# Optimization experiments

Measured on AMD Instinct MI355X. Metric: run time of the kernel, lower is better.

The kernel has to match this reference:

```python
import jax, jax.numpy as jnp
import numpy as np

T, B, N, DEG, F_IN, H, C = 48, 32, 96, 8, 16, 128, 500
E = B * N * DEG          # edges per timestep (already batch-offset within [0, B*N))
M = T * B * N            # total nodes across all timesteps
EPS = 1e-5               # BatchNorm eps


def setup_inputs() -> dict:
    key = jax.random.key(0)
    ks = jax.random.split(key, 24)
    rn = lambda k, s: jax.random.normal(k, s, dtype=jnp.float32) * 0.05
    return {
        "x": jax.random.normal(ks[0], (T, B * N, F_IN), dtype=jnp.float32),
        "edge_index": jax.random.randint(ks[1], (T, 2, E), 0, B * N, dtype=jnp.int32),
        "gcn_w0": rn(ks[2], (F_IN, H)),
        "gcn_w12": rn(ks[3], (2, H, H)),
        "gcn_b": rn(ks[4], (3, H)),
        "bn_gamma": jnp.ones((3, H), dtype=jnp.float32),
        "bn_beta": jnp.zeros((3, H), dtype=jnp.float32),
        "bn_mean": rn(ks[5], (3, H)),
        "bn_var": jax.random.uniform(ks[6], (3, H), minval=0.5, maxval=1.5, dtype=jnp.float32),
        "lstm_wih0": rn(ks[7], (2, 4 * H, H)),
        "lstm_whh0": rn(ks[8], (2, 4 * H, H)),
        "lstm_bih0": rn(ks[9], (2, 4 * H)),
        "lstm_bhh0": rn(ks[10], (2, 4 * H)),
        "lstm_wih1": rn(ks[11], (2, 4 * H, 2 * H)),
        "lstm_whh1": rn(ks[12], (2, 4 * H, H)),
        "lstm_bih1": rn(ks[13], (2, 4 * H)),
        "lstm_bhh1": rn(ks[14], (2, 4 * H)),
        "attn_w1": rn(ks[15], (2 * H, H)),
        "attn_b1": rn(ks[16], (H,)),
        "attn_w2": rn(ks[17], (H, 1)),
        "attn_b2": rn(ks[18], (1,)),
        "fc1_w": rn(ks[19], (2 * H, H)),
        "fc1_b": rn(ks[20], (H,)),
        "fc2_w": rn(ks[21], (H, C)),
        "fc2_b": rn(ks[22], (C,)),
    }


def _lstm_dir(x, wih, whh, bih, bhh):
    # x: [T, B, I]; PyTorch gate order i, f, g, o
    pre = jnp.einsum('tbi,gi->tbg', x, wih) + bih  # input projection hoisted out of scan
    h0 = jnp.zeros((x.shape[1], whh.shape[1]), x.dtype)

    def step(carry, p):
        h, c = carry
        g = p + h @ whh.T + bhh
        i, f, gg, o = jnp.split(g, 4, axis=-1)
        c = jax.nn.sigmoid(f) * c + jax.nn.sigmoid(i) * jnp.tanh(gg)
        h = jax.nn.sigmoid(o) * jnp.tanh(c)
        return (h, c), h

    _, hs = jax.lax.scan(step, (h0, h0), pre)
    return hs  # [T, B, Hh]


def _bilstm(x, wih, whh, bih, bhh):
    fwd = _lstm_dir(x, wih[0], whh[0], bih[0], bhh[0])
    bwd = _lstm_dir(x[::-1], wih[1], whh[1], bih[1], bhh[1])[::-1]
    return jnp.concatenate([fwd, bwd], axis=-1)  # [T, B, 2H]


def reference(x, edge_index, gcn_w0, gcn_w12, gcn_b,
              bn_gamma, bn_beta, bn_mean, bn_var,
              lstm_wih0, lstm_whh0, lstm_bih0, lstm_bhh0,
              lstm_wih1, lstm_whh1, lstm_bih1, lstm_bhh1,
              attn_w1, attn_b1, attn_w2, attn_b2,
              fc1_w, fc1_b, fc2_w, fc2_b):
    # Fold timesteps into one big node set by offsetting indices by t*B*N
    off = (jnp.arange(T, dtype=jnp.int32) * (B * N))[:, None]
    src = (edge_index[:, 0] + off).reshape(-1)
    dst = (edge_index[:, 1] + off).reshape(-1)

    # GCN symmetric norm with self-loops: deg counts incoming edges + self-loop
    deg = jax.ops.segment_sum(jnp.ones_like(src, dtype=x.dtype), dst, num_segments=M) + 1.0
    dinv = jax.lax.rsqrt(deg)
    enorm = (dinv[src] * dinv[dst])[:, None]   # per-edge norm
    self_norm = (1.0 / deg)[:, None]           # self-loop norm

    h = x.reshape(M, F_IN)
    for l in range(3):
        W = gcn_w0 if l == 0 else gcn_w12[l - 1]
        hw = h @ W  # GCNConv applies linear first
        z = jax.ops.segment_sum(hw[src] * enorm, dst, num_segments=M) + hw * self_norm + gcn_b[l]
        # BatchNorm1d eval-mode (running stats), then ReLU, residual if shapes match
        z = (z - bn_mean[l]) * (bn_gamma[l] * jax.lax.rsqrt(bn_var[l] + EPS)) + bn_beta[l]
        z = jax.nn.relu(z)
        h = z + h if l > 0 else z  # dropout is identity in eval

    # global_mean_pool per graph (fixed N nodes per graph)
    emb = h.reshape(T, B, N, H).mean(axis=2)  # [T, B, H]

    out1 = _bilstm(emb, lstm_wih0, lstm_whh0, lstm_bih0, lstm_bhh0)
    out2 = _bilstm(out1, lstm_wih1, lstm_whh1, lstm_bih1, lstm_bhh1)
    lstm_out = out2.transpose(1, 0, 2)  # [B, T, 2H]

    a = jnp.tanh(lstm_out @ attn_w1 + attn_b1) @ attn_w2 + attn_b2  # [B, T, 1]
    w = jax.nn.softmax(a, axis=1)
    ws = jnp.sum(lstm_out * w, axis=1)  # [B, 2H]

    y = jax.nn.relu(ws @ fc1_w + fc1_b) @ fc2_w + fc2_b
    return jax.nn.log_softmax(y, axis=1)
```

## Files before the change

### kernel.cpp

```cpp
#include <hip/hip_runtime.h>

#define T_ 48
#define B_ 32
#define N_ 96
#define E_ 24576
#define BN_ (B_*N_)
#define M_ (T_*BN_)
#define FIN_ 16
#define H_ 128
#define C_ 500
#define TE_ (T_*E_)
#define EPS_ 1e-5f

typedef _Float16 f16x8 __attribute__((ext_vector_type(8)));
typedef float    f32x4 __attribute__((ext_vector_type(4)));
typedef _Float16 half2v __attribute__((ext_vector_type(2)));

__device__ __forceinline__ ushort f2h(float f) {
    _Float16 h = (_Float16)f;
    union { _Float16 h; ushort u; } v;
    v.h = h;
    return v.u;
}
__device__ __forceinline__ float h2f(ushort u) {
    union { ushort u; _Float16 h; } v;
    v.u = u;
    return (float)v.h;
}
__device__ __forceinline__ half2v pkfma(unsigned int v, unsigned int w, half2v acc) {
#if __has_builtin(__builtin_elementwise_fma)
    return __builtin_elementwise_fma(__builtin_bit_cast(half2v, v),
                                     __builtin_bit_cast(half2v, w), acc);
#else
    half2v hv = __builtin_bit_cast(half2v, v);
    half2v wv = __builtin_bit_cast(half2v, w);
    acc[0] += hv[0]*wv[0];
    acc[1] += hv[1]*wv[1];
    return acc;
#endif
}
__device__ __forceinline__ float dot2pk(unsigned int hbits, unsigned int wbits, float acc) {
#if __has_builtin(__builtin_amdgcn_fdot2)
    return __builtin_amdgcn_fdot2(__builtin_bit_cast(half2v, hbits),
                                  __builtin_bit_cast(half2v, wbits), acc, false);
#else
    half2v hv = __builtin_bit_cast(half2v, hbits);
    half2v wv = __builtin_bit_cast(half2v, wbits);
    acc = fmaf((float)hv[0], (float)wv[0], acc);
    acc = fmaf((float)hv[1], (float)wv[1], acc);
    return acc;
#endif
}
__device__ __forceinline__ float sigm(float x) {
    return 1.f / (1.f + __expf(-x));
}
__device__ __forceinline__ float ftanh(float x) {
    x = fminf(15.f, fmaxf(-15.f, x));
    float e = __expf(2.f * x);
    return (e - 1.f) / (e + 1.f);
}

#define WPREP_TOTAL (384+1024+4096+16384+16384+65536+65536+131072+262144)
#define WPREP_BLOCKS ((WPREP_TOTAL + 1023) / 1024)
__global__ __launch_bounds__(1024) void csr_wprep_k(
    const int* __restrict__ ei, int* __restrict__ csr_off,
    unsigned int* __restrict__ csr_pk,
    const float* __restrict__ gcn_b, const float* __restrict__ gam,
    const float* __restrict__ bet, const float* __restrict__ mu,
    const float* __restrict__ var,
    float* __restrict__ bn_sc, float* __restrict__ bn_sh,
    const float* __restrict__ bih0, const float* __restrict__ bhh0,
    float* __restrict__ bias0,
    const float* __restrict__ bih1, const float* __restrict__ bhh1,
    float* __restrict__ bias1,
    const float* __restrict__ gcn_w0, const float* __restrict__ gcn_w12,
    ushort* __restrict__ w0t, ushort* __restrict__ w1t, ushort* __restrict__ w2t,
    const float* __restrict__ whh0, const float* __restrict__ whh1,
    unsigned int* __restrict__ wpk0, unsigned int* __restrict__ wpk1,
    const float* __restrict__ wih0, const float* __restrict__ wih1,
    ushort* __restrict__ wih0b, ushort* __restrict__ wih1b)
{
    __shared__ int cnt[BN_];
    __shared__ int cur[BN_];
    __shared__ int scanbuf[1024];
    __shared__ unsigned int pk[E_];
    int tid = threadIdx.x;

    if (blockIdx.x >= T_) {
        int i = (blockIdx.x - T_) * 1024 + tid;
        if (i >= WPREP_TOTAL) return;
        if (i < 384) {
            float sc = gam[i] * rsqrtf(var[i] + EPS_);
            bn_sc[i] = sc;
            bn_sh[i] = gcn_b[i]*sc + bet[i] - mu[i]*sc;
            return;
        }
        i -= 384;
        if (i < 1024) {
            bias0[i] = bih0[i] + bhh0[i];
            bias1[i] = bih1[i] + bhh1[i];
            return;
        }
        i -= 1024;
        if (i < 4096) {
            int e = i & 7, lane = (i >> 3) & 63, ct = i >> 9;
            int k = (lane >> 4)*8 + e;
            int c = ct*16 + (lane & 15);
            w0t[i] = (k < 16) ? f2h(gcn_w0[k*128 + c]) : (ushort)0;
            return;
        }
        i -= 4096;
        if (i < 16384) {
            int e = i & 7, lane = (i >> 3) & 63, kk = (i >> 9) & 3, ct = i >> 11;
            int k = kk*32 + (lane >> 4)*8 + e;
            int c = ct*16 + (lane & 15);
            w1t[i] = f2h(gcn_w12[k*128 + c]);
            return;
        }
        i -= 16384;
        if (i < 16384) {
            int e = i & 7, lane = (i >> 3) & 63, kk = (i >> 9) & 3, ct = i >> 11;
            int k = kk*32 + (lane >> 4)*8 + e;
            int c = ct*16 + (lane & 15);
            w2t[i] = f2h(gcn_w12[16384 + k*128 + c]);
            return;
        }
        i -= 16384;
        if (i < 65536) {
            int dir = i >> 15, r = i & 32767;
            int ab = r >> 14, r2 = r & 16383;
            int q = r2 >> 8, tidw = r2 & 255;
            int hh = tidw >> 1, gp = tidw & 1;
            int g = (2*gp + ab)*128 + hh;
            const float* wr = whh0 + ((long)(dir*512 + g))*128 + 2*q;
            wpk0[i] = (unsigned int)f2h(wr[0]) | ((unsigned int)f2h(wr[1]) << 16);
            return;
        }
        i -= 65536;
        if (i < 65536) {
            int dir = i >> 15, r = i & 32767;
            int ab = r >> 14, r2 = r & 16383;
            int q = r2 >> 8, tidw = r2 & 255;
            int hh = tidw >> 1, gp = tidw & 1;
            int g = (2*gp + ab)*128 + hh;
            const float* wr = whh1 + ((long)(dir*512 + g))*128 + 2*q;
            wpk1[i] = (unsigned int)f2h(wr[0]) | ((unsigned int)f2h(wr[1]) << 16);
            return;
        }
        i -= 65536;
        if (i < 131072) {
            int dir = i >> 16, r = i & 0xFFFF;
            int nt = r >> 11, kk = (r >> 9) & 3, lane = (r >> 3) & 63, e = r & 7;
            int n = nt*16 + (lane & 15);
            int k = kk*32 + (lane >> 4)*8 + e;
            wih0b[i] = f2h(wih0[((long)dir*512 + n)*128 + k]);
            return;
        }
        i -= 131072;
        {
            int dir = i >> 17, r = i & 0x1FFFF;
            int nt = r >> 12, kk = (r >> 9) & 7, lane = (r >> 3) & 63, e = r & 7;
            int n = nt*16 + (lane & 15);
            int k = kk*32 + (lane >> 4)*8 + e;
            wih1b[i] = f2h(wih1[((long)dir*512 + n)*256 + k]);
        }
        return;
    }

    int t = blockIdx.x;

    #pragma unroll
    for (int i = 0; i < 3; i++) cnt[tid + i*1024] = 0;
    __syncthreads();

    const int* srcp = ei + ((long)t*2+0)*E_;
    const int* dstp = ei + ((long)t*2+1)*E_;
    #pragma unroll
    for (int i = 0; i < E_/1024; i++)
        atomicAdd(&cnt[dstp[tid + i*1024]], 1);
    __syncthreads();

    int n0 = tid*3;
    int a = cnt[n0], b = cnt[n0+1], c = cnt[n0+2];
    int tot = a + b + c;
    scanbuf[tid] = tot;
    __syncthreads();
    for (int d = 1; d < 1024; d <<= 1) {
        int add = (tid >= d) ? scanbuf[tid-d] : 0;
        __syncthreads();
        scanbuf[tid] += add;
        __syncthreads();
    }
    int excl = scanbuf[tid] - tot;
    cur[n0] = excl; cur[n0+1] = excl + a; cur[n0+2] = excl + a + b;
    int gbase = t*BN_, ebase = t*E_;
    csr_off[gbase+n0]   = ebase + excl;
    csr_off[gbase+n0+1] = ebase + excl + a;
    csr_off[gbase+n0+2] = ebase + excl + a + b;
    if (t == T_-1 && tid == 0) csr_off[M_] = TE_;
    __syncthreads();

    #pragma unroll
    for (int i = 0; i < E_/1024; i++) {
        int e = tid + i*1024;
        int s = srcp[e], d = dstp[e];
        int pos = atomicAdd(&cur[d], 1);
        float w = rsqrtf((float)cnt[s] + 1.f) * rsqrtf((float)cnt[d] + 1.f);
        pk[pos] = (unsigned int)s | ((unsigned int)f2h(w) << 16);
    }
    __syncthreads();

    uint4* dpk = (uint4*)(csr_pk + ebase);
    const uint4* spk = (const uint4*)pk;
    #pragma unroll
    for (int i = 0; i < E_/4096; i++)
        dpk[tid + i*1024] = spk[tid + i*1024];
}

__global__ __launch_bounds__(512) void gcn_layer_k(
    const ushort* __restrict__ h, const ushort* __restrict__ Wt,
    ushort* __restrict__ Cout,
    const int* __restrict__ csr_off, const unsigned int* __restrict__ csr_pk,
    const float* __restrict__ bnsc, const float* __restrict__ bnsh)
{
    __shared__ ushort agg[64][136];
    int nb = gridDim.x;
    int chunk = nb >> 3;
    int bswz = (blockIdx.x & 7) * chunk + (blockIdx.x >> 3);
    int base = bswz * 64;
    int tbase = (base / BN_) * BN_;
    int wv = threadIdx.x >> 6;
    int lane = threadIdx.x & 63;
    int l2 = lane * 2;

    #pragma unroll
    for (int pass = 0; pass < 4; pass++) {
        int nlA = pass*16 + wv*2;
        int nodeA = __builtin_amdgcn_readfirstlane(base + nlA);
        int e00 = __builtin_amdgcn_readfirstlane(csr_off[nodeA]);
        int e01 = __builtin_amdgcn_readfirstlane(csr_off[nodeA+1]);
        int e11 = __builtin_amdgcn_readfirstlane(csr_off[nodeA+2]);
        int dA = e01 - e00, dB = e11 - e01;
        unsigned int mypkA = (lane < dA) ? csr_pk[e00 + lane] : 0u;
        unsigned int mypkB = (lane < dB) ? csr_pk[e01 + lane] : 0u;
        unsigned int selfA = *(const unsigned int*)(h + (size_t)nodeA*128 + l2);
        unsigned int selfB = *(const unsigned int*)(h + (size_t)(nodeA+1)*128 + l2);

        ushort swA = f2h(1.0f / (float)(dA + 1));
        ushort swB = f2h(1.0f / (float)(dB + 1));
        half2v spA = __builtin_bit_cast(half2v, (unsigned int)(swA * 0x10001u));
        half2v spB = __builtin_bit_cast(half2v, (unsigned int)(swB * 0x10001u));
        half2v a0 = __builtin_bit_cast(half2v, selfA);
        a0[0] *= spA[0]; a0[1] *= spA[1];
        half2v b0 = __builtin_bit_cast(half2v, selfB);
        b0[0] *= spB[0]; b0[1] *= spB[1];
        half2v a1 = {(_Float16)0.f, (_Float16)0.f}, a2 = a1, a3 = a1;
        half2v b1 = a1, b2 = a1, b3 = a1;

        int cA = (dA < 64) ? dA : 64;
        int cB = (dB < 64) ? dB : 64;
        int cA4 = cA & ~3, cB4 = cB & ~3;
        int cm = (cA4 > cB4) ? cA4 : cB4;
        for (int j = 0; j < cm; j += 4) {
            unsigned int pA0, pA1, pA2, pA3, vA0, vA1, vA2, vA3;
            unsigned int pB0, pB1, pB2, pB3, vB0, vB1, vB2, vB3;
            bool qA = (j < cA4), qB = (j < cB4);
            if (qA) {
                pA0 = (unsigned int)__builtin_amdgcn_readlane((int)mypkA, j+0);
                pA1 = (unsigned int)__builtin_amdgcn_readlane((int)mypkA, j+1);
                pA2 = (unsigned int)__builtin_amdgcn_readlane((int)mypkA, j+2);
                pA3 = (unsigned int)__builtin_amdgcn_readlane((int)mypkA, j+3);
                vA0 = *(const unsigned int*)(h + (size_t)(tbase + (int)(pA0 & 0xffffu))*128 + l2);
                vA1 = *(const unsigned int*)(h + (size_t)(tbase + (int)(pA1 & 0xffffu))*128 + l2);
                vA2 = *(const unsigned int*)(h + (size_t)(tbase + (int)(pA2 & 0xffffu))*128 + l2);
                vA3 = *(const unsigned int*)(h + (size_t)(tbase + (int)(pA3 & 0xffffu))*128 + l2);
            }
            if (qB) {
                pB0 = (unsigned int)__builtin_amdgcn_readlane((int)mypkB, j+0);
                pB1 = (unsigned int)__builtin_amdgcn_readlane((int)mypkB, j+1);
                pB2 = (unsigned int)__builtin_amdgcn_readlane((int)mypkB, j+2);
                pB3 = (unsigned int)__builtin_amdgcn_readlane((int)mypkB, j+3);
                vB0 = *(const unsigned int*)(h + (size_t)(tbase + (int)(pB0 & 0xffffu))*128 + l2);
                vB1 = *(const unsigned int*)(h + (size_t)(tbase + (int)(pB1 & 0xffffu))*128 + l2);
                vB2 = *(const unsigned int*)(h + (size_t)(tbase + (int)(pB2 & 0xffffu))*128 + l2);
                vB3 = *(const unsigned int*)(h + (size_t)(tbase + (int)(pB3 & 0xffffu))*128 + l2);
            }
            if (qA) {
                a0 = pkfma(vA0, (pA0 >> 16) * 0x10001u, a0);
                a1 = pkfma(vA1, (pA1 >> 16) * 0x10001u, a1);
                a2 = pkfma(vA2, (pA2 >> 16) * 0x10001u, a2);
                a3 = pkfma(vA3, (pA3 >> 16) * 0x10001u, a3);
            }
            if (qB) {
                b0 = pkfma(vB0, (pB0 >> 16) * 0x10001u, b0);
                b1 = pkfma(vB1, (pB1 >> 16) * 0x10001u, b1);
                b2 = pkfma(vB2, (pB2 >> 16) * 0x10001u, b2);
                b3 = pkfma(vB3, (pB3 >> 16) * 0x10001u, b3);
            }
        }
        for (int j = cA4; j < cA; j++) {
            unsigned int pk0 = (unsigned int)__builtin_amdgcn_readlane((int)mypkA, j);
            unsigned int v = *(const unsigned int*)(h + (size_t)(tbase + (int)(pk0 & 0xffffu))*128 + l2);
            a0 = pkfma(v, (pk0 >> 16) * 0x10001u, a0);
        }
        for (int j = cB4; j < cB; j++) {
            unsigned int pk0 = (unsigned int)__builtin_amdgcn_readlane((int)mypkB, j);
            unsigned int v = *(const unsigned int*)(h + (size_t)(tbase + (int)(pk0 & 0xffffu))*128 + l2);
            b0 = pkfma(v, (pk0 >> 16) * 0x10001u, b0);
        }
        for (int jj = e00 + 64; jj < e01; jj++) {
            unsigned int pk0 = __builtin_amdgcn_readfirstlane(csr_pk[jj]);
            unsigned int v = *(const unsigned int*)(h + (size_t)(tbase + (int)(pk0 & 0xffffu))*128 + l2);
            a0 = pkfma(v, (pk0 >> 16) * 0x10001u, a0);
        }
        for (int jj = e01 + 64; jj < e11; jj++) {
            unsigned int pk0 = __builtin_amdgcn_readfirstlane(csr_pk[jj]);
            unsigned int v = *(const unsigned int*)(h + (size_t)(tbase + (int)(pk0 & 0xffffu))*128 + l2);
            b0 = pkfma(v, (pk0 >> 16) * 0x10001u, b0);
        }
        float ra0 = ((float)a0[0] + (float)a1[0]) + ((float)a2[0] + (float)a3[0]);
        float ra1 = ((float)a0[1] + (float)a1[1]) + ((float)a2[1] + (float)a3[1]);
        float rb0 = ((float)b0[0] + (float)b1[0]) + ((float)b2[0] + (float)b3[0]);
        float rb1 = ((float)b0[1] + (float)b1[1]) + ((float)b2[1] + (float)b3[1]);
        *(unsigned int*)&agg[nlA][l2] =
            (unsigned int)f2h(ra0) | ((unsigned int)f2h(ra1) << 16);
        *(unsigned int*)&agg[nlA+1][l2] =
            (unsigned int)f2h(rb0) | ((unsigned int)f2h(rb1) << 16);
    }
    __syncthreads();

    int l16 = lane & 15, lh = lane >> 4;
    int rowgrp = wv >> 1;
    int chalf = (wv & 1) * 4;
    f32x4 acc[4];
    #pragma unroll
    for (int i = 0; i < 4; i++) acc[i] = (f32x4){0.f, 0.f, 0.f, 0.f};
    #pragma unroll
    for (int kk = 0; kk < 4; kk++) {
        f16x8 af = *reinterpret_cast<const f16x8*>(&agg[rowgrp*16 + l16][kk*32 + lh*8]);
        #pragma unroll
        for (int c4 = 0; c4 < 4; c4++) {
            int ct = chalf + c4;
            f16x8 bfr = *reinterpret_cast<const f16x8*>(
                &Wt[(((long)ct*4 + kk)*64 + lane)*8]);
            acc[c4] = __builtin_amdgcn_mfma_f32_16x16x32_f16(af, bfr, acc[c4], 0, 0, 0);
        }
    }
    __syncthreads();

    #pragma unroll
    for (int c4 = 0; c4 < 4; c4++) {
        int col = (chalf + c4)*16 + l16;
        float sc = bnsc[col], sh = bnsh[col];
        #pragma unroll
        for (int r = 0; r < 4; r++) {
            int rl = rowgrp*16 + lh*4 + r;
            float v = acc[c4][r] * sc + sh;
            agg[rl][col] = f2h(fmaxf(v, 0.f));
        }
    }
    __syncthreads();
    long rowblock = (long)base;
    #pragma unroll
    for (int it = 0; it < 2; it++) {
        int s = it*512 + threadIdx.x;
        int rl = s >> 4, c8 = (s & 15) * 8;
        uint4 v = *(const uint4*)&agg[rl][c8];
        uint4 rv = *(const uint4*)&h[(rowblock + rl)*128 + c8];
        half2v* vv = (half2v*)&v;
        const half2v* rr = (const half2v*)&rv;
        vv[0] += rr[0]; vv[1] += rr[1]; vv[2] += rr[2]; vv[3] += rr[3];
        *(uint4*)&Cout[(rowblock + rl)*128 + c8] = v;
    }
}

__global__ __launch_bounds__(256) void gcn0_k(
    const float* __restrict__ x, const ushort* __restrict__ Wt,
    ushort* __restrict__ Cout,
    const int* __restrict__ csr_off, const unsigned int* __restrict__ csr_pk,
    const float* __restrict__ bnsc, const float* __restrict__ bnsh)
{
    __shared__ ushort agg[64][32];
    __shared__ ushort cl[64][136];
    int tid = threadIdx.x;
    int nl = tid >> 2;
    int fq = tid & 3;
    int f0 = fq*4;
    int node = blockIdx.x*64 + nl;
    int tbase = (node / BN_) * BN_;
    int e0 = csr_off[node], e1 = csr_off[node+1];
    float s = 1.0f / (float)(e1 - e0 + 1);
    float4 sv = *(const float4*)(x + (long)node*16 + f0);
    float a0 = sv.x*s, a1 = sv.y*s, a2 = sv.z*s, a3 = sv.w*s;
    int j = e0;
    for (; j + 4 <= e1; j += 4) {
        unsigned int p0 = csr_pk[j], p1 = csr_pk[j+1], p2 = csr_pk[j+2], p3 = csr_pk[j+3];
        int s0 = tbase + (int)(p0 & 0xffffu), s1 = tbase + (int)(p1 & 0xffffu);
        int s2 = tbase + (int)(p2 & 0xffffu), s3 = tbase + (int)(p3 & 0xffffu);
        float w0 = h2f((ushort)(p0 >> 16)), w1 = h2f((ushort)(p1 >> 16));
        float w2 = h2f((ushort)(p2 >> 16)), w3 = h2f((ushort)(p3 >> 16));
        float4 v0 = *(const float4*)(x + (long)s0*16 + f0);
        float4 v1 = *(const float4*)(x + (long)s1*16 + f0);
        float4 v2 = *(const float4*)(x + (long)s2*16 + f0);
        float4 v3 = *(const float4*)(x + (long)s3*16 + f0);
        a0 += v0.x*w0 + v1.x*w1 + v2.x*w2 + v3.x*w3;
        a1 += v0.y*w0 + v1.y*w1 + v2.y*w2 + v3.y*w3;
        a2 += v0.z*w0 + v1.z*w1 + v2.z*w2 + v3.z*w3;
        a3 += v0.w*w0 + v1.w*w1 + v2.w*w2 + v3.w*w3;
    }
    for (; j < e1; j++) {
        unsigned int pk0 = csr_pk[j];
        int sc = tbase + (int)(pk0 & 0xffffu);
        float en = h2f((ushort)(pk0 >> 16));
        float4 v = *(const float4*)(x + (long)sc*16 + f0);
        a0 += v.x*en; a1 += v.y*en; a2 += v.z*en; a3 += v.w*en;
    }
    agg[nl][f0+0] = f2h(a0);
    agg[nl][f0+1] = f2h(a1);
    agg[nl][f0+2] = f2h(a2);
    agg[nl][f0+3] = f2h(a3);
    agg[nl][16+f0+0] = 0;
    agg[nl][16+f0+1] = 0;
    agg[nl][16+f0+2] = 0;
    agg[nl][16+f0+3] = 0;
    __syncthreads();

    int w = tid >> 6, lane = tid & 63;
    int l16 = lane & 15, lh = lane >> 4;
    f16x8 af = *reinterpret_cast<const f16x8*>(&agg[w*16 + l16][lh*8]);
    f32x4 acc[8];
    #pragma unroll
    for (int i = 0; i < 8; i++) acc[i] = (f32x4){0.f, 0.f, 0.f, 0.f};
    #pragma unroll
    for (int ct = 0; ct < 8; ct++) {
        f16x8 bfr = *reinterpret_cast<const f16x8*>(&Wt[((long)ct*64 + lane)*8]);
        acc[ct] = __builtin_amdgcn_mfma_f32_16x16x32_f16(af, bfr, acc[ct], 0, 0, 0);
    }

    #pragma unroll
    for (int ct = 0; ct < 8; ct++) {
        int col = ct*16 + l16;
        float sc = bnsc[col], sh = bnsh[col];
        #pragma unroll
        for (int r = 0; r < 4; r++) {
            int rl = w*16 + lh*4 + r;
            float v = acc[ct][r] * sc + sh;
            cl[rl][col] = f2h(fmaxf(v, 0.f));
        }
    }
    __syncthreads();
    long rowblock = (long)blockIdx.x * 64;
    #pragma unroll
    for (int it = 0; it < 4; it++) {
        int ss = it*256 + tid;
        int rl = ss >> 4, c8 = (ss & 15) * 8;
        uint4 v = *(const uint4*)&cl[rl][c8];
        *(uint4*)&Cout[(rowblock + rl)*128 + c8] = v;
    }
}

template<int K>
__global__ __launch_bounds__(256) void mm_pre_k(
    const ushort* __restrict__ A, const ushort* __restrict__ Wt_all,
    float* __restrict__ Cout_all, const float* __restrict__ bias_all)
{
    constexpr int KST = K/32;
    int dir = blockIdx.z;
    const ushort* Wt = Wt_all + (size_t)dir * 512 * K;
    float* Cout = Cout_all + (size_t)dir * T_ * B_ * 512;
    const float* bias = bias_all + dir * 512;

    int tid = threadIdx.x;
    int w = tid >> 6, lane = tid & 63;
    int l16 = lane & 15, lh = lane >> 4;
    int row0 = blockIdx.x * 64 + w * 16;
    int nt0 = blockIdx.y * 8;

    f32x4 acc[8];
    #pragma unroll
    for (int i = 0; i < 8; i++) acc[i] = (f32x4){0.f, 0.f, 0.f, 0.f};

    #pragma unroll
    for (int kk = 0; kk < KST; kk++) {
        int ka = kk*32 + lh*8;
        f16x8 af = *reinterpret_cast<const f16x8*>(&A[(long)(row0 + l16)*K + ka]);
        #pragma unroll
        for (int ct = 0; ct < 8; ct++) {
            f16x8 bfr = *reinterpret_cast<const f16x8*>(
                &Wt[(((long)(nt0 + ct)*KST + kk)*64 + lane)*8]);
            acc[ct] = __builtin_amdgcn_mfma_f32_16x16x32_f16(af, bfr, acc[ct], 0, 0, 0);
        }
    }

    #pragma unroll
    for (int ct = 0; ct < 8; ct++) {
        int col = (nt0 + ct)*16 + l16;
        float bv = bias[col];
        int gate = col >> 7, hh = col & 127;
        int colp = (gate & 1)*256 + hh*2 + (gate >> 1);
        #pragma unroll
        for (int r = 0; r < 4; r++) {
            int row = row0 + lh*4 + r;
            Cout[(long)row*512 + colp] = acc[ct][r] + bv;
        }
    }
}


__global__ void meanpool_k(const ushort* __restrict__ h, ushort* __restrict__ embb) {
    int row = blockIdx.x;
    int t = row / B_, b = row - t*B_;
    int hh = threadIdx.x;
    const ushort* base = h + ((long)t*BN_ + b*N_)*H_ + hh;
    float acc = 0.f;
    for (int n = 0; n < N_; n++) acc += h2f(base[(long)n*H_]);
    embb[(long)row*H_ + hh] = f2h(acc * (1.f / N_));
}

__global__ __launch_bounds__(256) void lstm_scan_k(
    const float* __restrict__ pre,
    const unsigned int* __restrict__ wpkbuf,
    float* __restrict__ out,
    ushort* __restrict__ outb)
{
    int dir = blockIdx.x >> 5;
    int b   = blockIdx.x & 31;
    int tid = threadIdx.x;
    int gp  = tid & 1;
    int hh  = tid >> 1;

    __shared__ ushort hbuf[2][H_];
    ((ushort*)hbuf)[tid] = 0;
    float creg = 0.f;

    const unsigned int* wpA = wpkbuf + ((long)dir*2 + 0)*64*256;
    const unsigned int* wpB = wpkbuf + ((long)dir*2 + 1)*64*256;
    unsigned int wA[64], wB[64];
    #pragma unroll
    for (int q = 0; q < 64; q++) {
        wA[q] = wpA[q*256 + tid];
        wB[q] = wpB[q*256 + tid];
    }

    const float* pred = pre + (long)dir * T_ * B_ * 512;
    int t = dir ? (T_ - 1) : 0;
    int tstep = dir ? -1 : 1;
    float pvA = pred[(((long)t*B_ + b)*2 + 0)*256 + tid];
    float pvB = pred[(((long)t*B_ + b)*2 + 1)*256 + tid];
    __syncthreads();

    for (int st = 0; st < T_; st++) {
        int tn = t + tstep;
        tn = (tn < 0) ? 0 : ((tn >= T_) ? T_ - 1 : tn);
        float pvAn = pred[(((long)tn*B_ + b)*2 + 0)*256 + tid];
        float pvBn = pred[(((long)tn*B_ + b)*2 + 1)*256 + tid];

        const uint4* h4 = (const uint4*)hbuf[st & 1];
        float a0 = pvA, a1 = 0.f, a2 = 0.f, a3 = 0.f;
        float c0 = pvB, c1 = 0.f, c2 = 0.f, c3 = 0.f;
        #pragma unroll
        for (int jj = 0; jj < 16; jj++) {
            uint4 hv = h4[jj];
            a0 = dot2pk(hv.x, wA[jj*4+0], a0);
            a1 = dot2pk(hv.y, wA[jj*4+1], a1);
            a2 = dot2pk(hv.z, wA[jj*4+2], a2);
            a3 = dot2pk(hv.w, wA[jj*4+3], a3);
            c0 = dot2pk(hv.x, wB[jj*4+0], c0);
            c1 = dot2pk(hv.y, wB[jj*4+1], c1);
            c2 = dot2pk(hv.z, wB[jj*4+2], c2);
            c3 = dot2pk(hv.w, wB[jj*4+3], c3);
        }
        float sA = (a0 + a1) + (a2 + a3);
        float sB = (c0 + c1) + (c2 + c3);
        float oA = __shfl_xor(sA, 1, 64);
        float oB = __shfl_xor(sB, 1, 64);
        float ig = gp ? oA : sA;
        float fg = gp ? oB : sB;
        float gg = gp ? sA : oA;
        float og = gp ? sB : oB;
        float c = sigm(fg) * creg + sigm(ig) * ftanh(gg);
        float h = sigm(og) * ftanh(c);
        creg = c;
        if (gp == 0) {
            hbuf[(st + 1) & 1][hh] = f2h(h);
            long orow = ((long)t*B_ + b)*256 + dir*H_ + hh;
            if (out)  out[orow] = h;
            if (outb) outb[orow] = f2h(h);
        }
        __syncthreads();
        pvA = pvAn; pvB = pvBn;
        t = tn;
    }
}


__global__ __launch_bounds__(128) void attn_a_k(
    const ushort* __restrict__ out2, const float* __restrict__ w1,
    const float* __restrict__ b1, const float* __restrict__ w2,
    const float* __restrict__ b2v, float* __restrict__ a)
{
    int row = blockIdx.x;
    int j = threadIdx.x;
    const ushort* xr = out2 + (long)row * 256;
    float acc = b1[j];
    for (int k = 0; k < 256; k++) acc += h2f(xr[k]) * w1[k*128 + j];
    float u = tanhf(acc) * w2[j];
    __shared__ float red[128];
    red[j] = u;
    __syncthreads();
    for (int d = 64; d > 0; d >>= 1) {
        if (j < d) red[j] += red[j + d];
        __syncthreads();
    }
    if (j == 0) {
        int t = row / B_, b = row - t*B_;
        a[b*T_ + t] = red[0] + b2v[0];
    }
}

__global__ __launch_bounds__(256) void attn_pool_k(
    const ushort* __restrict__ out2, const float* __restrict__ a,
    float* __restrict__ wsv)
{
    int b = blockIdx.x;
    __shared__ float w[T_];
    if (threadIdx.x == 0) {
        float m = -1e30f;
        for (int t = 0; t < T_; t++) m = fmaxf(m, a[b*T_ + t]);
        float s = 0.f;
        for (int t = 0; t < T_; t++) { float e = __expf(a[b*T_ + t] - m); w[t] = e; s += e; }
        float inv = 1.f / s;
        for (int t = 0; t < T_; t++) w[t] *= inv;
    }
    __syncthreads();
    int h2 = threadIdx.x;
    float acc = 0.f;
    for (int t = 0; t < T_; t++) acc += w[t] * h2f(out2[((long)t*B_ + b)*256 + h2]);
    wsv[b*256 + h2] = acc;
}


__global__ __launch_bounds__(512) void head_k(
    const float* __restrict__ wsv, const float* __restrict__ w1,
    const float* __restrict__ b1, const float* __restrict__ w2,
    const float* __restrict__ b2, float* __restrict__ outp)
{
    int b = blockIdx.x;
    int tid = threadIdx.x;
    __shared__ float r[128];
    __shared__ float y[C_];
    __shared__ float red[512];
    if (tid < 128) {
        float acc = b1[tid];
        for (int k = 0; k < 256; k++) acc += wsv[b*256 + k] * w1[k*128 + tid];
        r[tid] = fmaxf(acc, 0.f);
    }
    __syncthreads();
    for (int c = tid; c < C_; c += 512) {
        float acc = b2[c];
        for (int k = 0; k < 128; k++) acc += r[k] * w2[k*C_ + c];
        y[c] = acc;
    }
    __syncthreads();
    float m = -1e30f;
    for (int c = tid; c < C_; c += 512) m = fmaxf(m, y[c]);
    red[tid] = m;
    __syncthreads();
    for (int d = 256; d > 0; d >>= 1) {
        if (tid < d) red[tid] = fmaxf(red[tid], red[tid + d]);
        __syncthreads();
    }
    m = red[0];
    __syncthreads();
    float s = 0.f;
    for (int c = tid; c < C_; c += 512) s += __expf(y[c] - m);
    red[tid] = s;
    __syncthreads();
    for (int d = 256; d > 0; d >>= 1) {
        if (tid < d) red[tid] += red[tid + d];
        __syncthreads();
    }
    float lse = m + logf(red[0]);
    for (int c = tid; c < C_; c += 512) outp[(long)b*C_ + c] = y[c] - lse;
}


extern "C" void kernel_launch(void* const* d_in, const int* in_sizes, int n_in,
                              void* d_out, int out_size, void* d_ws, size_t ws_size,
                              hipStream_t stream) {
    const float* x        = (const float*)d_in[0];
    const int*   ei       = (const int*)d_in[1];
    const float* gcn_w0   = (const float*)d_in[2];
    const float* gcn_w12  = (const float*)d_in[3];
    const float* gcn_b    = (const float*)d_in[4];
    const float* bn_gamma = (const float*)d_in[5];
    const float* bn_beta  = (const float*)d_in[6];
    const float* bn_mean  = (const float*)d_in[7];
    const float* bn_var   = (const float*)d_in[8];
    const float* wih0     = (const float*)d_in[9];
    const float* whh0     = (const float*)d_in[10];
    const float* bih0     = (const float*)d_in[11];
    const float* bhh0     = (const float*)d_in[12];
    const float* wih1     = (const float*)d_in[13];
    const float* whh1     = (const float*)d_in[14];
    const float* bih1     = (const float*)d_in[15];
    const float* bhh1     = (const float*)d_in[16];
    const float* attn_w1  = (const float*)d_in[17];
    const float* attn_b1  = (const float*)d_in[18];
    const float* attn_w2  = (const float*)d_in[19];
    const float* attn_b2  = (const float*)d_in[20];
    const float* fc1_w    = (const float*)d_in[21];
    const float* fc1_b    = (const float*)d_in[22];
    const float* fc2_w    = (const float*)d_in[23];
    const float* fc2_b    = (const float*)d_in[24];

    char* p = (char*)d_ws;
    auto alloc = [&](size_t bytes) {
        void* r = (void*)p;
        p += (bytes + 255) & ~(size_t)255;
        return r;
    };
    ushort* hbA    = (ushort*)alloc((size_t)M_*H_*2);
    ushort* hbB    = (ushort*)alloc((size_t)M_*H_*2);
    int*   csr_off = (int*)  alloc((size_t)(M_+1)*4);
    unsigned int* csr_pk = (unsigned int*)alloc((size_t)TE_*4);
    float* bn_sc   = (float*)alloc(384*4);
    float* bn_sh   = (float*)alloc(384*4);
    float* bias0   = (float*)alloc(1024*4);
    float* bias1   = (float*)alloc(1024*4);
    ushort* w0t    = (ushort*)alloc((size_t)4096*2);
    ushort* w1t    = (ushort*)alloc((size_t)16384*2);
    ushort* w2t    = (ushort*)alloc((size_t)16384*2);
    unsigned int* wpk0 = (unsigned int*)alloc((size_t)2*64*512*4);
    unsigned int* wpk1 = (unsigned int*)alloc((size_t)2*64*512*4);
    ushort* wih0b  = (ushort*)alloc((size_t)2*512*128*2);
    ushort* wih1b  = (ushort*)alloc((size_t)2*512*256*2);
    ushort* embb   = (ushort*)alloc((size_t)T_*B_*H_*2);
    float* pre     = (float*)alloc((size_t)2*T_*B_*512*4);
    ushort* out1b  = (ushort*)alloc((size_t)T_*B_*256*2);
    ushort* out2b  = (ushort*)alloc((size_t)T_*B_*256*2);
    float* attn_av = (float*)alloc((size_t)B_*T_*4);
    float* wsv     = (float*)alloc((size_t)B_*256*4);

    csr_wprep_k<<<T_ + WPREP_BLOCKS, 1024, 0, stream>>>(
        ei, csr_off, csr_pk,
        gcn_b, bn_gamma, bn_beta, bn_mean, bn_var, bn_sc, bn_sh,
        bih0, bhh0, bias0, bih1, bhh1, bias1,
        gcn_w0, gcn_w12, w0t, w1t, w2t,
        whh0, whh1, wpk0, wpk1,
        wih0, wih1, wih0b, wih1b);

    gcn0_k<<<M_/64, 256, 0, stream>>>(x, w0t, hbA, csr_off, csr_pk,
                                      bn_sc + 0, bn_sh + 0);
    gcn_layer_k<<<M_/64, 512, 0, stream>>>(hbA, w1t, hbB, csr_off, csr_pk,
                                           bn_sc + 128, bn_sh + 128);
    gcn_layer_k<<<M_/64, 512, 0, stream>>>(hbB, w2t, hbA, csr_off, csr_pk,
                                           bn_sc + 256, bn_sh + 256);

    meanpool_k<<<T_*B_, 128, 0, stream>>>(hbA, embb);

    mm_pre_k<128><<<dim3((T_*B_)/64, 4, 2), 256, 0, stream>>>(embb, wih0b, pre, bias0);
    lstm_scan_k<<<64, 256, 0, stream>>>(pre, wpk0, nullptr, out1b);

    mm_pre_k<256><<<dim3((T_*B_)/64, 4, 2), 256, 0, stream>>>(out1b, wih1b, pre, bias1);
    lstm_scan_k<<<64, 256, 0, stream>>>(pre, wpk1, nullptr, out2b);

    attn_a_k<<<T_*B_, 128, 0, stream>>>(out2b, attn_w1, attn_b1, attn_w2, attn_b2, attn_av);
    attn_pool_k<<<B_, 256, 0, stream>>>(out2b, attn_av, wsv);

    head_k<<<B_, 512, 0, stream>>>(wsv, fc1_w, fc1_b, fc2_w, fc2_b, (float*)d_out);
}
```

Baseline: 270.5 us.

## Fuse attention scoring, softmax pooling and classifier head into one kernel

```diff
diff --git a/kernel.cpp b/kernel.cpp
--- a/kernel.cpp
+++ b/kernel.cpp
@@ -593,72 +593,72 @@
     }
 }
 
-
-__global__ __launch_bounds__(128) void attn_a_k(
-    const ushort* __restrict__ out2, const float* __restrict__ w1,
-    const float* __restrict__ b1, const float* __restrict__ w2,
-    const float* __restrict__ b2v, float* __restrict__ a)
-{
-    int row = blockIdx.x;
-    int j = threadIdx.x;
-    const ushort* xr = out2 + (long)row * 256;
-    float acc = b1[j];
-    for (int k = 0; k < 256; k++) acc += h2f(xr[k]) * w1[k*128 + j];
-    float u = tanhf(acc) * w2[j];
-    __shared__ float red[128];
-    red[j] = u;
-    __syncthreads();
-    for (int d = 64; d > 0; d >>= 1) {
-        if (j < d) red[j] += red[j + d];
-        __syncthreads();
-    }
-    if (j == 0) {
-        int t = row / B_, b = row - t*B_;
-        a[b*T_ + t] = red[0] + b2v[0];
-    }
-}
-
-__global__ __launch_bounds__(256) void attn_pool_k(
-    const ushort* __restrict__ out2, const float* __restrict__ a,
-    float* __restrict__ wsv)
-{
-    int b = blockIdx.x;
-    __shared__ float w[T_];
-    if (threadIdx.x == 0) {
-        float m = -1e30f;
-        for (int t = 0; t < T_; t++) m = fmaxf(m, a[b*T_ + t]);
-        float s = 0.f;
-        for (int t = 0; t < T_; t++) { float e = __expf(a[b*T_ + t] - m); w[t] = e; s += e; }
-        float inv = 1.f / s;
-        for (int t = 0; t < T_; t++) w[t] *= inv;
-    }
-    __syncthreads();
-    int h2 = threadIdx.x;
-    float acc = 0.f;
-    for (int t = 0; t < T_; t++) acc += w[t] * h2f(out2[((long)t*B_ + b)*256 + h2]);
-    wsv[b*256 + h2] = acc;
-}
-
-
-__global__ __launch_bounds__(512) void head_k(
-    const float* __restrict__ wsv, const float* __restrict__ w1,
-    const float* __restrict__ b1, const float* __restrict__ w2,
-    const float* __restrict__ b2, float* __restrict__ outp)
+__global__ __launch_bounds__(512) void attn_head_k(
+    const ushort* __restrict__ out2,
+    const float* __restrict__ aw1, const float* __restrict__ ab1,
+    const float* __restrict__ aw2, const float* __restrict__ ab2,
+    const float* __restrict__ fw1, const float* __restrict__ fb1,
+    const float* __restrict__ fw2, const float* __restrict__ fb2,
+    float* __restrict__ outp)
 {
     int b = blockIdx.x;
     int tid = threadIdx.x;
+    __shared__ ushort xs[T_][256];
+    __shared__ float uu[T_][129];
+    __shared__ float wgt[T_];
+    __shared__ float ws[256];
     __shared__ float r[128];
     __shared__ float y[C_];
     __shared__ float red[512];
+
+    for (int s = tid; s < T_*32; s += 512) {
+        int t = s >> 5, q = s & 31;
+        ((uint4*)&xs[t][0])[q] = ((const uint4*)(out2 + ((long)t*B_ + b)*256))[q];
+    }
+    __syncthreads();
+
+    {
+        int j = tid & 127;
+        int t0 = tid >> 7;
+        float w2v = aw2[j];
+        for (int t = t0; t < T_; t += 4) {
+            float acc = ab1[j];
+            for (int k = 0; k < 256; k++)
+                acc += h2f(xs[t][k]) * aw1[k*128 + j];
+            uu[t][j] = tanhf(acc) * w2v;
+        }
+    }
+    __syncthreads();
+    if (tid < T_) {
+        float s = 0.f;
+        for (int j = 0; j < 128; j++) s += uu[tid][j];
+        wgt[tid] = s + ab2[0];
+    }
+    __syncthreads();
+    if (tid == 0) {
+        float m = -1e30f;
+        for (int t = 0; t < T_; t++) m = fmaxf(m, wgt[t]);
+        float s = 0.f;
+        for (int t = 0; t < T_; t++) { float e = __expf(wgt[t] - m); wgt[t] = e; s += e; }
+        float inv = 1.f / s;
+        for (int t = 0; t < T_; t++) wgt[t] *= inv;
+    }
+    __syncthreads();
+    if (tid < 256) {
+        float acc = 0.f;
+        for (int t = 0; t < T_; t++) acc += wgt[t] * h2f(xs[t][tid]);
+        ws[tid] = acc;
+    }
+    __syncthreads();
     if (tid < 128) {
-        float acc = b1[tid];
-        for (int k = 0; k < 256; k++) acc += wsv[b*256 + k] * w1[k*128 + tid];
+        float acc = fb1[tid];
+        for (int k = 0; k < 256; k++) acc += ws[k] * fw1[k*128 + tid];
         r[tid] = fmaxf(acc, 0.f);
     }
     __syncthreads();
     for (int c = tid; c < C_; c += 512) {
-        float acc = b2[c];
-        for (int k = 0; k < 128; k++) acc += r[k] * w2[k*C_ + c];
+        float acc = fb2[c];
+        for (int k = 0; k < 128; k++) acc += r[k] * fw2[k*C_ + c];
         y[c] = acc;
     }
     __syncthreads();
@@ -739,8 +739,6 @@
     float* pre     = (float*)alloc((size_t)2*T_*B_*512*4);
     ushort* out1b  = (ushort*)alloc((size_t)T_*B_*256*2);
     ushort* out2b  = (ushort*)alloc((size_t)T_*B_*256*2);
-    float* attn_av = (float*)alloc((size_t)B_*T_*4);
-    float* wsv     = (float*)alloc((size_t)B_*256*4);
 
     csr_wprep_k<<<T_ + WPREP_BLOCKS, 1024, 0, stream>>>(
         ei, csr_off, csr_pk,
@@ -765,8 +763,7 @@
     mm_pre_k<256><<<dim3((T_*B_)/64, 4, 2), 256, 0, stream>>>(out1b, wih1b, pre, bias1);
     lstm_scan_k<<<64, 256, 0, stream>>>(pre, wpk1, nullptr, out2b);
 
-    attn_a_k<<<T_*B_, 128, 0, stream>>>(out2b, attn_w1, attn_b1, attn_w2, attn_b2, attn_av);
-    attn_pool_k<<<B_, 256, 0, stream>>>(out2b, attn_av, wsv);
-
-    head_k<<<B_, 512, 0, stream>>>(wsv, fc1_w, fc1_b, fc2_w, fc2_b, (float*)d_out);
-}
+    attn_head_k<<<B_, 512, 0, stream>>>(out2b,
+        attn_w1, attn_b1, attn_w2, attn_b2,
+        fc1_w, fc1_b, fc2_w, fc2_b, (float*)d_out);
+}
```

After: 305.7 us. 13.0% more time.
